# Optimization experiments

Hardware: AMD Instinct MI355X
Metric: run time of the kernel (lower is better)

The kernel has to match this reference:

```python
import jax, jax.numpy as jnp
import numpy as np

N_Q_HEADS = 16
N_KV_HEADS = 4
HEAD_DIM = 64
GROUPS = N_Q_HEADS // N_KV_HEADS


def apply_rope(xq, xk, cos, sin):
    # xq: [B,S,Hq,D], xk: [B,S,Hkv,D]; cos/sin: [S, D/2]
    def rot(t):
        tr = t[..., 0::2]
        ti = t[..., 1::2]
        c = cos[None, :, None, :]
        s = sin[None, :, None, :]
        out_r = tr * c - ti * s
        out_i = tr * s + ti * c
        # interleave back: [..., D/2, 2] -> [..., D]
        return jnp.stack([out_r, out_i], axis=-1).reshape(t.shape)
    return rot(xq), rot(xk)


def setup_inputs() -> dict:
    key = jax.random.key(0)
    ks = jax.random.split(key, 8)
    B, S, DIM = 2, 2048, 1024
    x = jax.random.normal(ks[0], (B, S, DIM), jnp.float32)
    # RoPE frequencies (llama-style): theta_i = 10000^(-2i/D), angles = pos * theta
    inv_freq = 1.0 / (10000.0 ** (jnp.arange(0, HEAD_DIM, 2, dtype=jnp.float32) / HEAD_DIM))
    angles = jnp.arange(S, dtype=jnp.float32)[:, None] * inv_freq[None, :]  # [S, D/2]
    freqs_cos = jnp.cos(angles)
    freqs_sin = jnp.sin(angles)
    # additive causal mask [1,1,S,S]
    neg = jnp.float32(-1e9)
    mask = jnp.where(jnp.tril(jnp.ones((S, S), bool)), 0.0, neg)[None, None]
    scale = 0.02
    wq = jax.random.normal(ks[1], (DIM, N_Q_HEADS * HEAD_DIM), jnp.float32) * scale
    wk = jax.random.normal(ks[2], (DIM, N_KV_HEADS * HEAD_DIM), jnp.float32) * scale
    wv = jax.random.normal(ks[3], (DIM, N_KV_HEADS * HEAD_DIM), jnp.float32) * scale
    wo = jax.random.normal(ks[4], (DIM, DIM), jnp.float32) * scale
    return {"x": x, "start_pos": 0, "freqs_cos": freqs_cos, "freqs_sin": freqs_sin,
            "mask": mask, "wq": wq, "wk": wk, "wv": wv, "wo": wo}


def reference(x, start_pos, freqs_cos, freqs_sin, mask, wq, wk, wv, wo):
    B, S, DIM = x.shape
    xq = (x @ wq).reshape(B, S, N_Q_HEADS, HEAD_DIM)
    xk = (x @ wk).reshape(B, S, N_KV_HEADS, HEAD_DIM)
    xv = (x @ wv).reshape(B, S, N_KV_HEADS, HEAD_DIM)
    xq, xk = apply_rope(xq, xk, freqs_cos, freqs_sin)
    # seq_len > 1: prefill path, no KV-cache read. repeat_kv: expand kv heads by GROUPS.
    keys = jnp.repeat(xk, GROUPS, axis=2)    # [B,S,Hq,D]
    values = jnp.repeat(xv, GROUPS, axis=2)
    q = xq.transpose(0, 2, 1, 3)             # [B,H,S,D]
    k = keys.transpose(0, 2, 1, 3)
    v = values.transpose(0, 2, 1, 3)
    scores = jnp.einsum('bhqd,bhkd->bhqk', q, k) / jnp.sqrt(jnp.float32(HEAD_DIM))
    scores = scores + mask
    probs = jax.nn.softmax(scores, axis=-1)
    attn = jnp.einsum('bhqk,bhkd->bhqd', probs, v)  # [B,H,S,D]
    attn = attn.transpose(0, 2, 1, 3).reshape(B, S, DIM)
    return attn @ wo
```

## Files before the change

kernel.cpp:

```cpp
#include <hip/hip_runtime.h>

typedef __bf16 bf16_t;
typedef __bf16 bf16x8 __attribute__((ext_vector_type(8)));
typedef __bf16 bf16x4 __attribute__((ext_vector_type(4)));
typedef float f32x4 __attribute__((ext_vector_type(4)));
typedef float f32x16 __attribute__((ext_vector_type(16)));

#if __has_builtin(__builtin_amdgcn_exp2f)
#define EXP2F __builtin_amdgcn_exp2f
#else
#define EXP2F exp2f
#endif

#define BATCH 2
#define SEQ   2048
#define DIM   1024
#define NQH   16
#define NKVH  4
#define HD    64
#define ROWS  (BATCH*SEQ)
#define QKVN  1536
#define QSCALE 0.1803368801111f

static __device__ __forceinline__ void gld16(const bf16_t* g, bf16_t* l) {
    __builtin_amdgcn_global_load_lds((const __attribute__((address_space(1))) void*)g,
                                     (__attribute__((address_space(3))) void*)l,
                                     16, 0, 0);
}

__global__ __launch_bounds__(256) void cast_x_kernel(const float* __restrict__ x,
                                                     bf16_t* __restrict__ o) {
    size_t i = ((size_t)blockIdx.x * 256 + threadIdx.x) * 4;
    float4 v = *(const float4*)(x + i);
    bf16x4 r;
    r[0] = (bf16_t)v.x; r[1] = (bf16_t)v.y; r[2] = (bf16_t)v.z; r[3] = (bf16_t)v.w;
    *(bf16x4*)(o + i) = r;
}

__global__ __launch_bounds__(256) void transpose_w_all(const float* __restrict__ wq,
                                                       const float* __restrict__ wk,
                                                       const float* __restrict__ wv,
                                                       const float* __restrict__ wo,
                                                       bf16_t* __restrict__ WqkvT,
                                                       bf16_t* __restrict__ WoT) {
    int bid = blockIdx.x;
    const float* src; bf16_t* dst; int N, nt, kt2;
    if (bid < 256)      { src = wq; dst = WqkvT;                      N = 1024; int i = bid;       nt = i & 15; kt2 = i >> 4; }
    else if (bid < 320) { src = wk; dst = WqkvT + (size_t)1024*1024;  N = 256;  int i = bid - 256; nt = i & 3;  kt2 = i >> 2; }
    else if (bid < 384) { src = wv; dst = WqkvT + (size_t)1280*1024;  N = 256;  int i = bid - 320; nt = i & 3;  kt2 = i >> 2; }
    else                { src = wo; dst = WoT;                        N = 1024; int i = bid - 384; nt = i & 15; kt2 = i >> 4; }

    __shared__ float tile[64][65];
    int t = threadIdx.x;
    {
        int r = t >> 2, cb = (t & 3) * 16;
        const float* s = src + (size_t)(kt2 * 64 + r) * N + nt * 64 + cb;
#pragma unroll
        for (int j = 0; j < 16; j += 4) {
            float4 v = *(const float4*)(s + j);
            tile[r][cb + j + 0] = v.x; tile[r][cb + j + 1] = v.y;
            tile[r][cb + j + 2] = v.z; tile[r][cb + j + 3] = v.w;
        }
    }
    __syncthreads();
    {
        int n = t >> 2, kb = (t & 3) * 16;
        union { bf16_t h[16]; uint4 u[2]; } pk;
#pragma unroll
        for (int j = 0; j < 16; ++j) pk.h[j] = (bf16_t)tile[kb + j][n];
        bf16_t* d = dst + (size_t)(nt * 64 + n) * 1024 + kt2 * 64 + kb;
        ((uint4*)d)[0] = pk.u[0];
        ((uint4*)d)[1] = pk.u[1];
    }
}

__global__ __launch_bounds__(256, 2) void gemm_qkv_kernel(const bf16_t* __restrict__ A,
                                                          const bf16_t* __restrict__ Bt,
                                                          const float* __restrict__ fcos,
                                                          const float* __restrict__ fsin,
                                                          bf16_t* __restrict__ Qb,
                                                          bf16_t* __restrict__ Kb,
                                                          bf16_t* __restrict__ Vt) {
    const int K = 1024;
    __shared__ __align__(16) bf16_t As[128 * 32];
    __shared__ __align__(16) bf16_t Bs[128 * 32];
    int t = threadIdx.x;
    int w = t >> 6, L = t & 63, quad = L >> 4, l15 = L & 15;
    int wr = (w >> 1) * 64, wc = (w & 1) * 64;
    int bnb = blockIdx.x;
    int bn = bnb * 128, bm = blockIdx.y * 128;

    const bf16_t* Ag0 = A  + (size_t)(bm + w * 32 + (L >> 2)) * K + (L & 3) * 8;
    const bf16_t* Ag1 = Ag0 + (size_t)16 * K;
    const bf16_t* Bg0 = Bt + (size_t)(bn + w * 32 + (L >> 2)) * K + (L & 3) * 8;
    const bf16_t* Bg1 = Bg0 + (size_t)16 * K;
    bf16_t* Al = As + w * 1024;
    bf16_t* Bl = Bs + w * 1024;

    f32x4 acc[4][4] = {};

    for (int k0 = 0; k0 < K; k0 += 32) {
        __syncthreads();
        gld16(Ag0 + k0, Al);
        gld16(Ag1 + k0, Al + 512);
        gld16(Bg0 + k0, Bl);
        gld16(Bg1 + k0, Bl + 512);
        __syncthreads();

        bf16x8 a[4], b[4];
#pragma unroll
        for (int i = 0; i < 4; ++i) {
            a[i] = ((const bf16x8*)As)[(wr + 16 * i + l15) * 4 + quad];
            b[i] = ((const bf16x8*)Bs)[(wc + 16 * i + l15) * 4 + quad];
        }
#pragma unroll
        for (int i = 0; i < 4; ++i)
#pragma unroll
            for (int j = 0; j < 4; ++j)
                acc[i][j] = __builtin_amdgcn_mfma_f32_16x16x32_bf16(a[i], b[j], acc[i][j], 0, 0, 0);
    }

    int region = (bnb >= 10) ? 2 : (bnb >= 8) ? 1 : 0;
#pragma unroll
    for (int i = 0; i < 4; ++i) {
        int row0 = bm + wr + 16 * i + quad * 4;
        int b = row0 >> 11, s0 = row0 & 2047;
#pragma unroll
        for (int j = 0; j < 4; ++j) {
            int col = bn + wc + 16 * j + l15;
            if (region == 2) {
                int kvh = (col >> 6) - 20, d = col & 63;
                int kt = s0 >> 6, kl = s0 & 63;
                bf16x4 o;
#pragma unroll
                for (int r = 0; r < 4; ++r) o[r] = (bf16_t)acc[i][j][r];
                *(bf16x4*)(Vt + ((size_t)((b * NKVH + kvh) * 32 + kt)) * 4096
                              + ((kl >> 3) * 64 + d) * 8 + (kl & 7)) = o;
            } else {
                int d = col & 63, fi = d >> 1;
                int odd = col & 1;
#pragma unroll
                for (int r = 0; r < 4; ++r) {
                    int s = s0 + r;
                    float v = acc[i][j][r];
                    float p = __shfl_xor(v, 1);
                    float c = fcos[s * 32 + fi], sn = fsin[s * 32 + fi];
                    float o = odd ? (p * sn + v * c) : (v * c - p * sn);
                    if (region == 0) {
                        int h = col >> 6;
                        Qb[((size_t)((b * NQH + h) * SEQ + s)) * HD + d] = (bf16_t)(o * QSCALE);
                    } else {
                        int kvh = (col >> 6) - 16;
                        int kt = s >> 6, kl = s & 63;
                        Kb[((size_t)((b * NKVH + kvh) * 32 + kt)) * 4096
                           + ((d >> 3) * 64 + kl) * 8 + (d & 7)] = (bf16_t)o;
                    }
                }
            }
        }
    }
}

__global__ __launch_bounds__(256, 2) void gemm_bt_kernel(const bf16_t* __restrict__ A,
                                                         const bf16_t* __restrict__ Bt,
                                                         float* __restrict__ C,
                                                         int M, int N, int K) {
    __shared__ __align__(16) bf16_t As[128 * 32];
    __shared__ __align__(16) bf16_t Bs[128 * 32];
    int t = threadIdx.x;
    int w = t >> 6, L = t & 63, quad = L >> 4, l15 = L & 15;
    int wr = (w >> 1) * 64, wc = (w & 1) * 64;
    int bn = blockIdx.x * 128, bm = blockIdx.y * 128;

    const bf16_t* Ag0 = A  + (size_t)(bm + w * 32 + (L >> 2)) * K + (L & 3) * 8;
    const bf16_t* Ag1 = Ag0 + (size_t)16 * K;
    const bf16_t* Bg0 = Bt + (size_t)(bn + w * 32 + (L >> 2)) * K + (L & 3) * 8;
    const bf16_t* Bg1 = Bg0 + (size_t)16 * K;
    bf16_t* Al = As + w * 1024;
    bf16_t* Bl = Bs + w * 1024;

    f32x4 acc[4][4] = {};

    for (int k0 = 0; k0 < K; k0 += 32) {
        __syncthreads();
        gld16(Ag0 + k0, Al);
        gld16(Ag1 + k0, Al + 512);
        gld16(Bg0 + k0, Bl);
        gld16(Bg1 + k0, Bl + 512);
        __syncthreads();

        bf16x8 a[4], b[4];
#pragma unroll
        for (int i = 0; i < 4; ++i) {
            a[i] = ((const bf16x8*)As)[(wr + 16 * i + l15) * 4 + quad];
            b[i] = ((const bf16x8*)Bs)[(wc + 16 * i + l15) * 4 + quad];
        }
#pragma unroll
        for (int i = 0; i < 4; ++i)
#pragma unroll
            for (int j = 0; j < 4; ++j)
                acc[i][j] = __builtin_amdgcn_mfma_f32_16x16x32_bf16(a[i], b[j], acc[i][j], 0, 0, 0);
    }

#pragma unroll
    for (int i = 0; i < 4; ++i) {
        int row = bm + wr + 16 * i + quad * 4;
#pragma unroll
        for (int j = 0; j < 4; ++j) {
            int col = bn + wc + 16 * j + l15;
            float* cp = C + (size_t)row * N + col;
#pragma unroll
            for (int r = 0; r < 4; ++r)
                cp[(size_t)r * N] = acc[i][j][r];
        }
    }
}

__global__ __launch_bounds__(256, 4) void attn_kernel(const bf16_t* __restrict__ Qb,
                                                      const bf16_t* __restrict__ Kb,
                                                      const bf16_t* __restrict__ Vt,
                                                      bf16_t* __restrict__ Ob) {
    int u = blockIdx.x;
    int k4 = u >> 8, x = u & 255;
    int j = x >> 5, bh = x & 31, b = bh >> 4, h = bh & 15;
    int a = (k4 == 0) ? j : (k4 == 1) ? (15 - j) : (k4 == 2) ? (16 + j) : (31 - j);
    int kv = h >> 2;
    int t = threadIdx.x, w = t >> 6, lane = t & 63, hi = lane >> 5, l31 = lane & 31;
    int rowg = w & 1, parity = w >> 1;
    int q = 64 * a + 32 * rowg + l31;

    __shared__ float cO[2][32][64];
    __shared__ float cRS[2][32];

    const bf16_t* Ktile = Kb + ((size_t)((b * NKVH + kv) * 32)) * 4096;
    const bf16_t* Vtile = Vt + ((size_t)((b * NKVH + kv) * 32)) * 4096;
    const bf16_t* Qrow  = Qb + ((size_t)((b * NQH + h) * SEQ + q)) * HD;

    bf16x8 qf[4];
#pragma unroll
    for (int ks = 0; ks < 4; ++ks)
        qf[ks] = *(const bf16x8*)(Qrow + ks * 16 + hi * 8);

    f32x16 acc[2] = {};
    float rs = 0.f;

    for (int kt = parity; kt <= a; kt += 2) {
        const bf16_t* Kt = Ktile + (size_t)kt * 4096;
        const bf16_t* Vv = Vtile + (size_t)kt * 4096;

        f32x16 st[2];
#pragma unroll
        for (int kg = 0; kg < 2; ++kg) {
            f32x16 z = {};
#pragma unroll
            for (int ks = 0; ks < 4; ++ks) {
                bf16x8 ak = *(const bf16x8*)(Kt + ((ks * 2 + hi) * 64 + kg * 32 + l31) * 8);
                z = __builtin_amdgcn_mfma_f32_32x32x16_bf16(ak, qf[ks], z, 0, 0, 0);
            }
            st[kg] = z;
        }

        bool diag = (kt == a);
        uint2 pk[2][2][2];
#pragma unroll
        for (int c = 0; c < 2; ++c)
#pragma unroll
            for (int uu = 0; uu < 2; ++uu)
#pragma unroll
                for (int hh = 0; hh < 2; ++hh) {
                    bf16x4 g;
#pragma unroll
                    for (int jl = 0; jl < 4; ++jl) {
                        int r = 8 * uu + 4 * hh + jl;
                        float p = EXP2F(st[c][r]);
                        if (diag) {
                            int key = kt * 64 + 32 * c + 16 * uu + 8 * hh + 4 * hi + jl;
                            if (key > q) p = 0.f;
                        }
                        rs += p;
                        g[jl] = (bf16_t)p;
                    }
                    union { bf16x4 b4; uint2 u2; } cv; cv.b4 = g;
                    pk[c][uu][hh] = cv.u2;
                }

#pragma unroll
        for (int tt = 0; tt < 4; ++tt) {
            int uu = tt & 1, c = tt >> 1;
            uint2 keep = hi ? pk[c][uu][1] : pk[c][uu][0];
            uint2 send = hi ? pk[c][uu][0] : pk[c][uu][1];
            uint2 recv;
            recv.x = __shfl_xor(send.x, 32);
            recv.y = __shfl_xor(send.y, 32);
            union { uint4 u4; bf16x8 b8; } fr;
            fr.u4 = hi ? make_uint4(recv.x, recv.y, keep.x, keep.y)
                       : make_uint4(keep.x, keep.y, recv.x, recv.y);
#pragma unroll
            for (int dg = 0; dg < 2; ++dg) {
                bf16x8 av = *(const bf16x8*)(Vv + ((tt * 2 + hi) * 64 + dg * 32 + l31) * 8);
                acc[dg] = __builtin_amdgcn_mfma_f32_32x32x16_bf16(av, fr.b8, acc[dg], 0, 0, 0);
            }
        }
    }

    rs += __shfl_xor(rs, 32);

    if (parity == 1) {
#pragma unroll
        for (int dg = 0; dg < 2; ++dg)
#pragma unroll
            for (int r = 0; r < 16; ++r)
                cO[rowg][dg * 16 + r][lane] = acc[dg][r];
        if (hi == 0) cRS[rowg][l31] = rs;
    }
    __syncthreads();
    if (parity == 0) {
#pragma unroll
        for (int dg = 0; dg < 2; ++dg)
#pragma unroll
            for (int r = 0; r < 16; ++r)
                acc[dg][r] += cO[rowg][dg * 16 + r][lane];
        rs += cRS[rowg][l31];

        float rinv = 1.0f / rs;
        bf16_t* obase = Ob + (size_t)(b * SEQ + q) * DIM + h * HD;
#pragma unroll
        for (int dg = 0; dg < 2; ++dg)
#pragma unroll
            for (int g2 = 0; g2 < 4; ++g2) {
                bf16x4 o;
#pragma unroll
                for (int jl = 0; jl < 4; ++jl) o[jl] = (bf16_t)(acc[dg][4 * g2 + jl] * rinv);
                *(bf16x4*)(obase + 32 * dg + 8 * g2 + 4 * hi) = o;
            }
    }
}

extern "C" void kernel_launch(void* const* d_in, const int* in_sizes, int n_in,
                              void* d_out, int out_size, void* d_ws, size_t ws_size,
                              hipStream_t stream) {
    const float* x    = (const float*)d_in[0];
    const float* fcos = (const float*)d_in[2];
    const float* fsin = (const float*)d_in[3];
    const float* wq   = (const float*)d_in[5];
    const float* wk   = (const float*)d_in[6];
    const float* wv   = (const float*)d_in[7];
    const float* wo   = (const float*)d_in[8];
    float* out = (float*)d_out;

    char* ws = (char*)d_ws;
    bf16_t* Xb    = (bf16_t*)(ws + 0);
    bf16_t* Attnb = Xb;
    bf16_t* WqkvT = (bf16_t*)(ws + 8388608);
    bf16_t* WoT   = (bf16_t*)(ws + 11534336);
    bf16_t* Qb    = (bf16_t*)(ws + 13631488);
    bf16_t* Kb    = (bf16_t*)(ws + 22020096);
    bf16_t* Vt    = (bf16_t*)(ws + 24117248);

    cast_x_kernel<<<ROWS * DIM / 1024, 256, 0, stream>>>(x, Xb);
    transpose_w_all<<<640, 256, 0, stream>>>(wq, wk, wv, wo, WqkvT, WoT);

    gemm_qkv_kernel<<<dim3(QKVN / 128, ROWS / 128), 256, 0, stream>>>(Xb, WqkvT, fcos, fsin, Qb, Kb, Vt);

    attn_kernel<<<1024, 256, 0, stream>>>(Qb, Kb, Vt, Attnb);

    gemm_bt_kernel<<<dim3(DIM / 128, ROWS / 128), 256, 0, stream>>>(Attnb, WoT, out, ROWS, DIM, DIM);
}
```

Baseline: 202.4 us.

## Restructure attention to one wave per 32-row query block and merge prep kernels

The attention kernel changes from 256-thread blocks, where two waves split the key tiles by parity and combine results through LDS, to 64-thread single-wave blocks. Each block owns 32 query rows, walks all causal key tiles itself, and launches longest-first. The diagonal masking moves into a templated tile function, and V fragments are loaded ahead of the softmax. The x cast and the weight transpose are merged into one launch. This removes the LDS reduction and __syncthreads and one launch, but each wave now does the full serial loop and the same K/V tile is loaded by twice as many waves.

```diff
diff --git a/kernel.cpp b/kernel.cpp
--- a/kernel.cpp
+++ b/kernel.cpp
@@ -28,30 +28,30 @@
                                      16, 0, 0);
 }
 
-__global__ __launch_bounds__(256) void cast_x_kernel(const float* __restrict__ x,
-                                                     bf16_t* __restrict__ o) {
-    size_t i = ((size_t)blockIdx.x * 256 + threadIdx.x) * 4;
-    float4 v = *(const float4*)(x + i);
-    bf16x4 r;
-    r[0] = (bf16_t)v.x; r[1] = (bf16_t)v.y; r[2] = (bf16_t)v.z; r[3] = (bf16_t)v.w;
-    *(bf16x4*)(o + i) = r;
-}
-
-__global__ __launch_bounds__(256) void transpose_w_all(const float* __restrict__ wq,
-                                                       const float* __restrict__ wk,
-                                                       const float* __restrict__ wv,
-                                                       const float* __restrict__ wo,
-                                                       bf16_t* __restrict__ WqkvT,
-                                                       bf16_t* __restrict__ WoT) {
-    int bid = blockIdx.x;
+__global__ __launch_bounds__(256) void prep_kernel(const float* __restrict__ x,
+                                                   const float* __restrict__ wq,
+                                                   const float* __restrict__ wk,
+                                                   const float* __restrict__ wv,
+                                                   const float* __restrict__ wo,
+                                                   bf16_t* __restrict__ Xb,
+                                                   bf16_t* __restrict__ WqkvT,
+                                                   bf16_t* __restrict__ WoT) {
+    __shared__ float tile[64][65];
+    int t = threadIdx.x;
+    if (blockIdx.x < 4096) {
+        size_t i = ((size_t)blockIdx.x * 256 + t) * 4;
+        float4 v = *(const float4*)(x + i);
+        bf16x4 r;
+        r[0] = (bf16_t)v.x; r[1] = (bf16_t)v.y; r[2] = (bf16_t)v.z; r[3] = (bf16_t)v.w;
+        *(bf16x4*)(Xb + i) = r;
+        return;
+    }
+    int bid = blockIdx.x - 4096;
     const float* src; bf16_t* dst; int N, nt, kt2;
     if (bid < 256)      { src = wq; dst = WqkvT;                      N = 1024; int i = bid;       nt = i & 15; kt2 = i >> 4; }
     else if (bid < 320) { src = wk; dst = WqkvT + (size_t)1024*1024;  N = 256;  int i = bid - 256; nt = i & 3;  kt2 = i >> 2; }
     else if (bid < 384) { src = wv; dst = WqkvT + (size_t)1280*1024;  N = 256;  int i = bid - 320; nt = i & 3;  kt2 = i >> 2; }
     else                { src = wo; dst = WoT;                        N = 1024; int i = bid - 384; nt = i & 15; kt2 = i >> 4; }
-
-    __shared__ float tile[64][65];
-    int t = threadIdx.x;
     {
         int r = t >> 2, cb = (t & 3) * 16;
         const float* s = src + (size_t)(kt2 * 64 + r) * N + nt * 64 + cb;
@@ -216,21 +216,82 @@
     }
 }
 
-__global__ __launch_bounds__(256, 4) void attn_kernel(const bf16_t* __restrict__ Qb,
-                                                      const bf16_t* __restrict__ Kb,
-                                                      const bf16_t* __restrict__ Vt,
-                                                      bf16_t* __restrict__ Ob) {
-    int u = blockIdx.x;
-    int k4 = u >> 8, x = u & 255;
-    int j = x >> 5, bh = x & 31, b = bh >> 4, h = bh & 15;
-    int a = (k4 == 0) ? j : (k4 == 1) ? (15 - j) : (k4 == 2) ? (16 + j) : (31 - j);
+template <bool DIAG>
+static __device__ __forceinline__ void attn_tile(const bf16_t* __restrict__ Kt,
+                                                 const bf16_t* __restrict__ Vv,
+                                                 const bf16x8* qf, int q, int kt,
+                                                 int hi, int l31,
+                                                 f32x16* acc, float& rs) {
+    f32x16 st[2];
+#pragma unroll
+    for (int kg = 0; kg < 2; ++kg) {
+        f32x16 z = {};
+#pragma unroll
+        for (int ks = 0; ks < 4; ++ks) {
+            bf16x8 ak = *(const bf16x8*)(Kt + ((ks * 2 + hi) * 64 + kg * 32 + l31) * 8);
+            z = __builtin_amdgcn_mfma_f32_32x32x16_bf16(ak, qf[ks], z, 0, 0, 0);
+        }
+        st[kg] = z;
+    }
+
+    bf16x8 av[4][2];
+#pragma unroll
+    for (int tt = 0; tt < 4; ++tt)
+#pragma unroll
+        for (int dg = 0; dg < 2; ++dg)
+            av[tt][dg] = *(const bf16x8*)(Vv + ((tt * 2 + hi) * 64 + dg * 32 + l31) * 8);
+
+    uint2 pk[2][2][2];
+#pragma unroll
+    for (int c = 0; c < 2; ++c)
+#pragma unroll
+        for (int uu = 0; uu < 2; ++uu)
+#pragma unroll
+            for (int hh = 0; hh < 2; ++hh) {
+                bf16x4 g;
+#pragma unroll
+                for (int jl = 0; jl < 4; ++jl) {
+                    int r = 8 * uu + 4 * hh + jl;
+                    float p = EXP2F(st[c][r]);
+                    if (DIAG) {
+                        int key = kt * 64 + 32 * c + 16 * uu + 8 * hh + 4 * hi + jl;
+                        if (key > q) p = 0.f;
+                    }
+                    rs += p;
+                    g[jl] = (bf16_t)p;
+                }
+                union { bf16x4 b4; uint2 u2; } cv; cv.b4 = g;
+                pk[c][uu][hh] = cv.u2;
+            }
+
+#pragma unroll
+    for (int tt = 0; tt < 4; ++tt) {
+        int uu = tt & 1, c = tt >> 1;
+        uint2 keep = hi ? pk[c][uu][1] : pk[c][uu][0];
+        uint2 send = hi ? pk[c][uu][0] : pk[c][uu][1];
+        uint2 recv;
+        recv.x = __shfl_xor(send.x, 32);
+        recv.y = __shfl_xor(send.y, 32);
+        union { uint4 u4; bf16x8 b8; } fr;
+        fr.u4 = hi ? make_uint4(recv.x, recv.y, keep.x, keep.y)
+                   : make_uint4(keep.x, keep.y, recv.x, recv.y);
+#pragma unroll
+        for (int dg = 0; dg < 2; ++dg)
+            acc[dg] = __builtin_amdgcn_mfma_f32_32x32x16_bf16(av[tt][dg], fr.b8, acc[dg], 0, 0, 0);
+    }
+}
+
+__global__ __launch_bounds__(64, 4) void attn_kernel(const bf16_t* __restrict__ Qb,
+                                                     const bf16_t* __restrict__ Kb,
+                                                     const bf16_t* __restrict__ Vt,
+                                                     bf16_t* __restrict__ Ob) {
+    int bid = blockIdx.x;
+    int g = 63 - (bid >> 5);
+    int bh = bid & 31, b = bh >> 4, h = bh & 15;
     int kv = h >> 2;
-    int t = threadIdx.x, w = t >> 6, lane = t & 63, hi = lane >> 5, l31 = lane & 31;
-    int rowg = w & 1, parity = w >> 1;
-    int q = 64 * a + 32 * rowg + l31;
-
-    __shared__ float cO[2][32][64];
-    __shared__ float cRS[2][32];
+    int lane = threadIdx.x & 63, hi = lane >> 5, l31 = lane & 31;
+    int q = 32 * g + l31;
+    int ntiles = (g >> 1) + 1;
 
     const bf16_t* Ktile = Kb + ((size_t)((b * NKVH + kv) * 32)) * 4096;
     const bf16_t* Vtile = Vt + ((size_t)((b * NKVH + kv) * 32)) * 4096;
@@ -244,96 +305,27 @@
     f32x16 acc[2] = {};
     float rs = 0.f;
 
-    for (int kt = parity; kt <= a; kt += 2) {
-        const bf16_t* Kt = Ktile + (size_t)kt * 4096;
-        const bf16_t* Vv = Vtile + (size_t)kt * 4096;
-
-        f32x16 st[2];
-#pragma unroll
-        for (int kg = 0; kg < 2; ++kg) {
-            f32x16 z = {};
-#pragma unroll
-            for (int ks = 0; ks < 4; ++ks) {
-                bf16x8 ak = *(const bf16x8*)(Kt + ((ks * 2 + hi) * 64 + kg * 32 + l31) * 8);
-                z = __builtin_amdgcn_mfma_f32_32x32x16_bf16(ak, qf[ks], z, 0, 0, 0);
-            }
-            st[kg] = z;
-        }
-
-        bool diag = (kt == a);
-        uint2 pk[2][2][2];
-#pragma unroll
-        for (int c = 0; c < 2; ++c)
-#pragma unroll
-            for (int uu = 0; uu < 2; ++uu)
-#pragma unroll
-                for (int hh = 0; hh < 2; ++hh) {
-                    bf16x4 g;
-#pragma unroll
-                    for (int jl = 0; jl < 4; ++jl) {
-                        int r = 8 * uu + 4 * hh + jl;
-                        float p = EXP2F(st[c][r]);
-                        if (diag) {
-                            int key = kt * 64 + 32 * c + 16 * uu + 8 * hh + 4 * hi + jl;
-                            if (key > q) p = 0.f;
-                        }
-                        rs += p;
-                        g[jl] = (bf16_t)p;
-                    }
-                    union { bf16x4 b4; uint2 u2; } cv; cv.b4 = g;
-                    pk[c][uu][hh] = cv.u2;
-                }
-
-#pragma unroll
-        for (int tt = 0; tt < 4; ++tt) {
-            int uu = tt & 1, c = tt >> 1;
-            uint2 keep = hi ? pk[c][uu][1] : pk[c][uu][0];
-            uint2 send = hi ? pk[c][uu][0] : pk[c][uu][1];
-            uint2 recv;
-            recv.x = __shfl_xor(send.x, 32);
-            recv.y = __shfl_xor(send.y, 32);
-            union { uint4 u4; bf16x8 b8; } fr;
-            fr.u4 = hi ? make_uint4(recv.x, recv.y, keep.x, keep.y)
-                       : make_uint4(keep.x, keep.y, recv.x, recv.y);
-#pragma unroll
-            for (int dg = 0; dg < 2; ++dg) {
-                bf16x8 av = *(const bf16x8*)(Vv + ((tt * 2 + hi) * 64 + dg * 32 + l31) * 8);
-                acc[dg] = __builtin_amdgcn_mfma_f32_32x32x16_bf16(av, fr.b8, acc[dg], 0, 0, 0);
-            }
-        }
+    for (int kt = 0; kt < ntiles - 1; ++kt)
+        attn_tile<false>(Ktile + (size_t)kt * 4096, Vtile + (size_t)kt * 4096,
+                         qf, q, kt, hi, l31, acc, rs);
+    {
+        int kt = ntiles - 1;
+        attn_tile<true>(Ktile + (size_t)kt * 4096, Vtile + (size_t)kt * 4096,
+                        qf, q, kt, hi, l31, acc, rs);
     }
 
     rs += __shfl_xor(rs, 32);
-
-    if (parity == 1) {
-#pragma unroll
-        for (int dg = 0; dg < 2; ++dg)
-#pragma unroll
-            for (int r = 0; r < 16; ++r)
-                cO[rowg][dg * 16 + r][lane] = acc[dg][r];
-        if (hi == 0) cRS[rowg][l31] = rs;
-    }
-    __syncthreads();
-    if (parity == 0) {
-#pragma unroll
-        for (int dg = 0; dg < 2; ++dg)
-#pragma unroll
-            for (int r = 0; r < 16; ++r)
-                acc[dg][r] += cO[rowg][dg * 16 + r][lane];
-        rs += cRS[rowg][l31];
-
-        float rinv = 1.0f / rs;
-        bf16_t* obase = Ob + (size_t)(b * SEQ + q) * DIM + h * HD;
-#pragma unroll
-        for (int dg = 0; dg < 2; ++dg)
-#pragma unroll
-            for (int g2 = 0; g2 < 4; ++g2) {
-                bf16x4 o;
-#pragma unroll
-                for (int jl = 0; jl < 4; ++jl) o[jl] = (bf16_t)(acc[dg][4 * g2 + jl] * rinv);
-                *(bf16x4*)(obase + 32 * dg + 8 * g2 + 4 * hi) = o;
-            }
-    }
+    float rinv = 1.0f / rs;
+    bf16_t* obase = Ob + (size_t)(b * SEQ + q) * DIM + h * HD;
+#pragma unroll
+    for (int dg = 0; dg < 2; ++dg)
+#pragma unroll
+        for (int g2 = 0; g2 < 4; ++g2) {
+            bf16x4 o;
+#pragma unroll
+            for (int jl = 0; jl < 4; ++jl) o[jl] = (bf16_t)(acc[dg][4 * g2 + jl] * rinv);
+            *(bf16x4*)(obase + 32 * dg + 8 * g2 + 4 * hi) = o;
+        }
 }
 
 extern "C" void kernel_launch(void* const* d_in, const int* in_sizes, int n_in,
@@ -357,12 +349,11 @@
     bf16_t* Kb    = (bf16_t*)(ws + 22020096);
     bf16_t* Vt    = (bf16_t*)(ws + 24117248);
 
-    cast_x_kernel<<<ROWS * DIM / 1024, 256, 0, stream>>>(x, Xb);
-    transpose_w_all<<<640, 256, 0, stream>>>(wq, wk, wv, wo, WqkvT, WoT);
+    prep_kernel<<<4096 + 640, 256, 0, stream>>>(x, wq, wk, wv, wo, Xb, WqkvT, WoT);
 
     gemm_qkv_kernel<<<dim3(QKVN / 128, ROWS / 128), 256, 0, stream>>>(Xb, WqkvT, fcos, fsin, Qb, Kb, Vt);
 
-    attn_kernel<<<1024, 256, 0, stream>>>(Qb, Kb, Vt, Attnb);
+    attn_kernel<<<2048, 64, 0, stream>>>(Qb, Kb, Vt, Attnb);
 
     gemm_bt_kernel<<<dim3(DIM / 128, ROWS / 128), 256, 0, stream>>>(Attnb, WoT, out, ROWS, DIM, DIM);
 }
```

Result: slower. 224.7 us (+11.0%).
